# Kernel tuning notes

Hardware: AMD Instinct MI355X
Metric: run time of the kernel (lower is better)

Reference implementation:

```python
import jax, jax.numpy as jnp
import numpy as np

B, S, D, H, O = 64, 512, 1024, 1024, 1024


def setup_inputs() -> dict:
    key = jax.random.key(0)
    ks = jax.random.split(key, 7)
    s_in = 1.0 / np.sqrt(D)
    s_h = 1.0 / np.sqrt(H)
    return {
        "x": jax.random.normal(ks[0], (B, S, D), dtype=jnp.float32),
        # gate order along axis 0: i, f, o, c_candidate
        "Wx": jax.random.uniform(ks[1], (4, H, D), jnp.float32, -s_in, s_in),
        "bx": jax.random.uniform(ks[2], (4, H), jnp.float32, -s_in, s_in),
        "Wh": jax.random.uniform(ks[3], (4, H, H), jnp.float32, -s_h, s_h),
        "bh": jax.random.uniform(ks[4], (4, H), jnp.float32, -s_h, s_h),
        "Wp": jax.random.uniform(ks[5], (O, H), jnp.float32, -s_h, s_h),
        "bp": jax.random.uniform(ks[6], (O,), jnp.float32, -s_h, s_h),
    }


def reference(x, Wx, bx, Wh, bh, Wp, bp):
    b, s, d = x.shape
    h_dim = Wh.shape[-1]
    # Precompute all input-to-hidden gate projections in one big GEMM:
    # equivalent to W_i(x_t)+b, W_f(x_t)+b, W_o(x_t)+b, W_c(x_t)+b per step.
    xg = jnp.einsum('bsd,ghd->sbgh', x, Wx) + bx  # [S, B, 4, H]

    def step(carry, xg_t):
        c, h = carry
        # hidden-to-hidden projections for all 4 gates, fused
        g = xg_t + jnp.einsum('bh,gkh->bgk', h, Wh) + bh  # [B, 4, H]
        i = jax.nn.sigmoid(g[:, 0])
        f = jax.nn.sigmoid(g[:, 1])
        o = jax.nn.sigmoid(g[:, 2])
        c_cand = jnp.tanh(g[:, 3])
        c_new = f * c + i * c_cand
        h_new = o * jnp.tanh(c_new)
        y = h_new @ Wp.T + bp  # [B, O]
        return (c_new, h_new), y

    init = (jnp.zeros((b, h_dim), x.dtype), jnp.zeros((b, h_dim), x.dtype))
    (c, h), ys = jax.lax.scan(step, init, xg)
    outputs = jnp.transpose(ys, (1, 0, 2))  # [B, S, O]
    return outputs, (c, h)
```

## Files before the change

kernel.cpp:

```cpp
#include <hip/hip_runtime.h>


typedef unsigned short u16;
typedef u16   u16x4  __attribute__((ext_vector_type(4)));
typedef u16   u16x8  __attribute__((ext_vector_type(8)));
typedef __bf16 bf16x8 __attribute__((ext_vector_type(8)));
typedef float f32x4  __attribute__((ext_vector_type(4)));

__device__ __forceinline__ u16 f2bf(float x) {
    unsigned u = __float_as_uint(x);
    u = (u + 0x7FFFu + ((u >> 16) & 1u)) >> 16;
    return (u16)u;
}
__device__ __forceinline__ float bf2f(u16 h) {
    return __uint_as_float(((unsigned)h) << 16);
}
__device__ __forceinline__ float fsig(float x) { return 1.f / (1.f + __expf(-x)); }
__device__ __forceinline__ float ftanh(float x) { return 1.f - 2.f / (__expf(2.f * x) + 1.f); }


__global__ void k_convert_x(const float* __restrict__ x, u16* __restrict__ xb) {
    int bi = blockIdx.x;
    int b = bi >> 9, s = bi & 511;
    const float4* src = (const float4*)(x + (size_t)bi * 1024);
    u16* dst = xb + ((size_t)(s * 64 + b)) * 1024;
    int t = threadIdx.x;
    float4 v = src[t];
    u16x4 o; o.x = f2bf(v.x); o.y = f2bf(v.y); o.z = f2bf(v.z); o.w = f2bf(v.w);
    *(u16x4*)(dst + t * 4) = o;
}

__global__ void k_pack_gates(const float* __restrict__ w, u16* __restrict__ wp) {
    int np = blockIdx.x;
    int g = np & 3, k = np >> 2;
    const float4* src = (const float4*)(w + ((size_t)(g * 1024 + k)) * 1024);
    u16* dst = wp + (size_t)np * 1024;
    int t = threadIdx.x;
    float4 v = src[t];
    u16x4 o; o.x = f2bf(v.x); o.y = f2bf(v.y); o.z = f2bf(v.z); o.w = f2bf(v.w);
    *(u16x4*)(dst + t * 4) = o;
}

__global__ void k_f2bf(const float* __restrict__ src, u16* __restrict__ dst, int n) {
    int i = (blockIdx.x * 256 + threadIdx.x) * 4;
    if (i < n) {
        float4 v = *(const float4*)(src + i);
        u16x4 o; o.x = f2bf(v.x); o.y = f2bf(v.y); o.z = f2bf(v.z); o.w = f2bf(v.w);
        *(u16x4*)(dst + i) = o;
    }
}

__global__ void k_bias(const float* __restrict__ bx, const float* __restrict__ bh,
                       float* __restrict__ bias) {
    int np = blockIdx.x * 256 + threadIdx.x;
    int g = np & 3, k = np >> 2;
    bias[np] = bx[g * 1024 + k] + bh[g * 1024 + k];
}

__global__ void k_init(u16* __restrict__ hall0, float* __restrict__ cstate) {
    int i = blockIdx.x * 256 + threadIdx.x;
    hall0[i] = 0;
    cstate[i] = 0.f;
}

__global__ __launch_bounds__(256) void k_gemm64(
    const u16* __restrict__ A, const u16* __restrict__ Bt,
    int K, int N, int mode,
    u16* __restrict__ Cb,
    float* __restrict__ Cf, const float* __restrict__ bp, int S_, int O_) {
    __shared__ u16 As[64 * 72];
    __shared__ u16 Bs[64 * 72];
    int mb = blockIdx.x, nb = blockIdx.y;
    int tid = threadIdx.x, w = tid >> 6, lane = tid & 63;
    f32x4 acc[4] = {};
    int kchunks = K >> 6;
    for (int kc = 0; kc < kchunks; ++kc) {
        int k0 = kc * 64;
#pragma unroll
        for (int r = 0; r < 2; ++r) {
            int c = tid + 256 * r;
            int row = c >> 3, kk = (c & 7) * 8;
            *(u16x8*)(&As[row * 72 + kk]) =
                *(const u16x8*)(A + (size_t)(mb * 64 + row) * K + k0 + kk);
            *(u16x8*)(&Bs[row * 72 + kk]) =
                *(const u16x8*)(Bt + (size_t)(nb * 64 + row) * K + k0 + kk);
        }
        __syncthreads();
#pragma unroll
        for (int kk = 0; kk < 64; kk += 32) {
            bf16x8 a = *(const bf16x8*)(&As[(w * 16 + (lane & 15)) * 72 + kk + (lane >> 4) * 8]);
#pragma unroll
            for (int nt = 0; nt < 4; ++nt) {
                bf16x8 b = *(const bf16x8*)(&Bs[(nt * 16 + (lane & 15)) * 72 + kk + (lane >> 4) * 8]);
                acc[nt] = __builtin_amdgcn_mfma_f32_16x16x32_bf16(a, b, acc[nt], 0, 0, 0);
            }
        }
        __syncthreads();
    }
    int q = lane >> 4, cl = lane & 15;
    if (mode == 0) {
#pragma unroll
        for (int nt = 0; nt < 4; ++nt)
#pragma unroll
            for (int j = 0; j < 4; ++j) {
                int m = mb * 64 + w * 16 + q * 4 + j;
                int n = nb * 64 + nt * 16 + cl;
                Cb[(size_t)m * N + n] = f2bf(acc[nt][j]);
            }
    } else {
#pragma unroll
        for (int nt = 0; nt < 4; ++nt)
#pragma unroll
            for (int j = 0; j < 4; ++j) {
                int m = mb * 64 + w * 16 + q * 4 + j;
                int n = nb * 64 + nt * 16 + cl;
                int b = m & 63, s = m >> 6;
                Cf[((size_t)b * S_ + s) * O_ + n] = acc[nt][j] + bp[n];
            }
    }
}

__global__ __launch_bounds__(256) void k_step(
    const u16* __restrict__ hprev,
    const u16* __restrict__ whp,
    const u16* __restrict__ xgt,
    const float* __restrict__ bias,
    float* __restrict__ cstate,
    float* __restrict__ hf32,
    u16* __restrict__ hnext) {
    __shared__ u16 As[64 * 264];
    __shared__ u16 Bs[16 * 264];
    __shared__ float glds[64 * 20];
    int nb = blockIdx.x;
    int tid = threadIdx.x, w = tid >> 6, lane = tid & 63;
    f32x4 acc = {};
    for (int kc = 0; kc < 4; ++kc) {
        int k0 = kc * 256;
#pragma unroll
        for (int r = 0; r < 8; ++r) {
            int c = tid + 256 * r;
            int row = c >> 5, kk = (c & 31) * 8;
            *(u16x8*)(&As[row * 264 + kk]) =
                *(const u16x8*)(hprev + (size_t)row * 1024 + k0 + kk);
        }
#pragma unroll
        for (int r = 0; r < 2; ++r) {
            int c = tid + 256 * r;
            int row = c >> 5, kk = (c & 31) * 8;
            *(u16x8*)(&Bs[row * 264 + kk]) =
                *(const u16x8*)(whp + (size_t)(nb * 16 + row) * 1024 + k0 + kk);
        }
        __syncthreads();
#pragma unroll
        for (int kk = 0; kk < 256; kk += 32) {
            bf16x8 a = *(const bf16x8*)(&As[(w * 16 + (lane & 15)) * 264 + kk + (lane >> 4) * 8]);
            bf16x8 b = *(const bf16x8*)(&Bs[(lane & 15) * 264 + kk + (lane >> 4) * 8]);
            acc = __builtin_amdgcn_mfma_f32_16x16x32_bf16(a, b, acc, 0, 0, 0);
        }
        __syncthreads();
    }
    int q = lane >> 4, cl = lane & 15;
#pragma unroll
    for (int j = 0; j < 4; ++j) {
        int row = w * 16 + q * 4 + j;
        int n = nb * 16 + cl;
        glds[row * 20 + cl] = acc[j] + bf2f(xgt[(size_t)row * 4096 + n]) + bias[n];
    }
    __syncthreads();
    {
        int row = tid >> 2, kv = tid & 3;
        float4 gv = *(const float4*)(&glds[row * 20 + kv * 4]);
        float ig = fsig(gv.x), fg = fsig(gv.y), og = fsig(gv.z), cc = ftanh(gv.w);
        int k = nb * 4 + kv;
        float c_old = cstate[row * 1024 + k];
        float c_new = fg * c_old + ig * cc;
        cstate[row * 1024 + k] = c_new;
        float h = og * ftanh(c_new);
        hf32[row * 1024 + k] = h;
        hnext[row * 1024 + k] = f2bf(h);
    }
}

__global__ void k_tail(const float* __restrict__ cstate, const float* __restrict__ hf32,
                       float* __restrict__ out) {
    int i = blockIdx.x * 256 + threadIdx.x;
    if (i < 65536) out[33554432 + i] = cstate[i];
    else           out[33554432 + i] = hf32[i - 65536];
}

extern "C" void kernel_launch(void* const* d_in, const int* in_sizes, int n_in,
                              void* d_out, int out_size, void* d_ws, size_t ws_size,
                              hipStream_t stream) {
    const float* x  = (const float*)d_in[0];
    const float* Wx = (const float*)d_in[1];
    const float* bx = (const float*)d_in[2];
    const float* Wh = (const float*)d_in[3];
    const float* bh = (const float*)d_in[4];
    const float* Wp = (const float*)d_in[5];
    const float* bp = (const float*)d_in[6];
    float* out = (float*)d_out;
    char* ws = (char*)d_ws;

    u16*   xb   = (u16*)  (ws);
    u16*   wxp  = (u16*)  (ws + 67108864);
    u16*   whp  = (u16*)  (ws + 75497472);
    u16*   wpb  = (u16*)  (ws + 83886080);
    float* bias = (float*)(ws + 85983232);
    float* cst  = (float*)(ws + 85999616);
    float* hf32 = (float*)(ws + 86261760);
    u16*   xg   = (u16*)  (ws + 86523904);
    u16*   hall = (u16*)  (ws + 354959360);

    k_convert_x<<<32768, 256, 0, stream>>>(x, xb);
    k_pack_gates<<<4096, 256, 0, stream>>>(Wx, wxp);
    k_pack_gates<<<4096, 256, 0, stream>>>(Wh, whp);
    k_f2bf<<<1024, 256, 0, stream>>>(Wp, wpb, 1048576);
    k_bias<<<16, 256, 0, stream>>>(bx, bh, bias);
    k_init<<<256, 256, 0, stream>>>(hall, cst);

    k_gemm64<<<dim3(512, 64), 256, 0, stream>>>(xb, wxp, 1024, 4096, 0,
                                                xg, nullptr, nullptr, 0, 0);
    for (int t = 0; t < 512; ++t) {
        k_step<<<256, 256, 0, stream>>>(hall + (size_t)t * 65536, whp,
                                        xg + (size_t)t * 64 * 4096, bias,
                                        cst, hf32, hall + (size_t)(t + 1) * 65536);
    }
    k_gemm64<<<dim3(512, 16), 256, 0, stream>>>(hall + 65536, wpb, 1024, 1024, 1,
                                                nullptr, out, bp, 512, 1024);
    k_tail<<<512, 256, 0, stream>>>(cst, hf32, out);
}
```

Measured before the change: 4.963 ms.

## Replace per-step LSTM launches with persistent cooperative kernel and grid barrier

Replaces the 512 per-timestep kernel launches with one cooperative persistent kernel of 256 blocks that loops over time and synchronises through a global atomic barrier. Each block keeps its slice of the recurrent weights resident in LDS for the whole run, and cell state stays in registers. The hidden state is read straight from global memory into the MFMA operands instead of being staged through LDS. This removes launch overhead and repeated weight reloads, but adds grid-barrier latency and spin contention on a single counter, and relies on all blocks being co-resident.

```diff
diff --git a/kernel.cpp b/kernel.cpp
--- a/kernel.cpp
+++ b/kernel.cpp
@@ -57,10 +57,12 @@
     bias[np] = bx[g * 1024 + k] + bh[g * 1024 + k];
 }
 
-__global__ void k_init(u16* __restrict__ hall0, float* __restrict__ cstate) {
+__global__ void k_init(u16* __restrict__ hall0, float* __restrict__ cstate,
+                       unsigned* __restrict__ bar) {
     int i = blockIdx.x * 256 + threadIdx.x;
     hall0[i] = 0;
     cstate[i] = 0.f;
+    if (i < 4) bar[i] = 0u;
 }
 
 __global__ __launch_bounds__(256) void k_gemm64(
@@ -120,65 +122,80 @@
     }
 }
 
-__global__ __launch_bounds__(256) void k_step(
-    const u16* __restrict__ hprev,
+__global__ __launch_bounds__(256) void k_recur(
     const u16* __restrict__ whp,
-    const u16* __restrict__ xgt,
+    const u16* __restrict__ xg,
     const float* __restrict__ bias,
-    float* __restrict__ cstate,
+    u16* __restrict__ hall,
+    float* __restrict__ cst,
     float* __restrict__ hf32,
-    u16* __restrict__ hnext) {
-    __shared__ u16 As[64 * 264];
-    __shared__ u16 Bs[16 * 264];
+    unsigned* __restrict__ bar) {
+    __shared__ u16 Bs[16 * 1032];
     __shared__ float glds[64 * 20];
     int nb = blockIdx.x;
     int tid = threadIdx.x, w = tid >> 6, lane = tid & 63;
-    f32x4 acc = {};
-    for (int kc = 0; kc < 4; ++kc) {
-        int k0 = kc * 256;
-#pragma unroll
-        for (int r = 0; r < 8; ++r) {
-            int c = tid + 256 * r;
-            int row = c >> 5, kk = (c & 31) * 8;
-            *(u16x8*)(&As[row * 264 + kk]) =
-                *(const u16x8*)(hprev + (size_t)row * 1024 + k0 + kk);
-        }
-#pragma unroll
-        for (int r = 0; r < 2; ++r) {
-            int c = tid + 256 * r;
-            int row = c >> 5, kk = (c & 31) * 8;
-            *(u16x8*)(&Bs[row * 264 + kk]) =
-                *(const u16x8*)(whp + (size_t)(nb * 16 + row) * 1024 + k0 + kk);
-        }
-        __syncthreads();
-#pragma unroll
-        for (int kk = 0; kk < 256; kk += 32) {
-            bf16x8 a = *(const bf16x8*)(&As[(w * 16 + (lane & 15)) * 264 + kk + (lane >> 4) * 8]);
-            bf16x8 b = *(const bf16x8*)(&Bs[(lane & 15) * 264 + kk + (lane >> 4) * 8]);
+    int q = lane >> 4, cl = lane & 15;
+
+#pragma unroll
+    for (int r = 0; r < 8; ++r) {
+        int c = tid + 256 * r;
+        int row = c >> 7, kk = (c & 127) * 8;
+        *(u16x8*)(&Bs[row * 1032 + kk]) =
+            *(const u16x8*)(whp + (size_t)(nb * 16 + row) * 1024 + kk);
+    }
+    float bcol = bias[nb * 16 + cl];
+    int grow = tid >> 2, gkv = tid & 3;
+    int gk = nb * 4 + gkv;
+    float c_reg = 0.f, h_last = 0.f;
+    __syncthreads();
+
+    for (int t = 0; t < 512; ++t) {
+        const u16* xgt = xg + (size_t)t * 64 * 4096;
+        int row0 = w * 16 + q * 4;
+        int ncol = nb * 16 + cl;
+        u16 xv0 = xgt[(size_t)(row0 + 0) * 4096 + ncol];
+        u16 xv1 = xgt[(size_t)(row0 + 1) * 4096 + ncol];
+        u16 xv2 = xgt[(size_t)(row0 + 2) * 4096 + ncol];
+        u16 xv3 = xgt[(size_t)(row0 + 3) * 4096 + ncol];
+        const u16* hrow = hall + (size_t)t * 65536 + (size_t)(w * 16 + cl) * 1024 + q * 8;
+        f32x4 acc = {};
+#pragma unroll
+        for (int kk = 0; kk < 1024; kk += 32) {
+            bf16x8 a = *(const bf16x8*)(hrow + kk);
+            bf16x8 b = *(const bf16x8*)(&Bs[cl * 1032 + kk + q * 8]);
             acc = __builtin_amdgcn_mfma_f32_16x16x32_bf16(a, b, acc, 0, 0, 0);
         }
-        __syncthreads();
-    }
-    int q = lane >> 4, cl = lane & 15;
-#pragma unroll
-    for (int j = 0; j < 4; ++j) {
-        int row = w * 16 + q * 4 + j;
-        int n = nb * 16 + cl;
-        glds[row * 20 + cl] = acc[j] + bf2f(xgt[(size_t)row * 4096 + n]) + bias[n];
-    }
-    __syncthreads();
-    {
-        int row = tid >> 2, kv = tid & 3;
-        float4 gv = *(const float4*)(&glds[row * 20 + kv * 4]);
+        glds[(row0 + 0) * 20 + cl] = acc[0] + bf2f(xv0) + bcol;
+        glds[(row0 + 1) * 20 + cl] = acc[1] + bf2f(xv1) + bcol;
+        glds[(row0 + 2) * 20 + cl] = acc[2] + bf2f(xv2) + bcol;
+        glds[(row0 + 3) * 20 + cl] = acc[3] + bf2f(xv3) + bcol;
+        __syncthreads();
+        float4 gv = *(const float4*)(&glds[grow * 20 + gkv * 4]);
         float ig = fsig(gv.x), fg = fsig(gv.y), og = fsig(gv.z), cc = ftanh(gv.w);
-        int k = nb * 4 + kv;
-        float c_old = cstate[row * 1024 + k];
-        float c_new = fg * c_old + ig * cc;
-        cstate[row * 1024 + k] = c_new;
-        float h = og * ftanh(c_new);
-        hf32[row * 1024 + k] = h;
-        hnext[row * 1024 + k] = f2bf(h);
-    }
+        c_reg = fg * c_reg + ig * cc;
+        h_last = og * ftanh(c_reg);
+        hall[(size_t)(t + 1) * 65536 + grow * 1024 + gk] = f2bf(h_last);
+        __syncthreads();
+        if (tid == 0) {
+            __builtin_amdgcn_fence(__ATOMIC_RELEASE, "agent");
+            unsigned p = (unsigned)t & 1u;
+            unsigned my = __hip_atomic_fetch_add(&bar[p], 1u, __ATOMIC_ACQ_REL,
+                                                 __HIP_MEMORY_SCOPE_AGENT);
+            if (my == 255u) {
+                __hip_atomic_store(&bar[p], 0u, __ATOMIC_RELAXED,
+                                   __HIP_MEMORY_SCOPE_AGENT);
+                __hip_atomic_fetch_add(&bar[2], 1u, __ATOMIC_RELEASE,
+                                       __HIP_MEMORY_SCOPE_AGENT);
+            } else {
+                while (__hip_atomic_load(&bar[2], __ATOMIC_ACQUIRE,
+                                         __HIP_MEMORY_SCOPE_AGENT) < (unsigned)(t + 1)) {}
+            }
+            __builtin_amdgcn_fence(__ATOMIC_ACQUIRE, "agent");
+        }
+        __syncthreads();
+    }
+    cst[grow * 1024 + gk] = c_reg;
+    hf32[grow * 1024 + gk] = h_last;
 }
 
 __global__ void k_tail(const float* __restrict__ cstate, const float* __restrict__ hf32,
@@ -201,29 +218,31 @@
     float* out = (float*)d_out;
     char* ws = (char*)d_ws;
 
-    u16*   xb   = (u16*)  (ws);
-    u16*   wxp  = (u16*)  (ws + 67108864);
-    u16*   whp  = (u16*)  (ws + 75497472);
-    u16*   wpb  = (u16*)  (ws + 83886080);
-    float* bias = (float*)(ws + 85983232);
-    float* cst  = (float*)(ws + 85999616);
-    float* hf32 = (float*)(ws + 86261760);
-    u16*   xg   = (u16*)  (ws + 86523904);
-    u16*   hall = (u16*)  (ws + 354959360);
+    u16*      xb   = (u16*)     (ws);
+    u16*      wxp  = (u16*)     (ws + 67108864);
+    u16*      whp  = (u16*)     (ws + 75497472);
+    u16*      wpb  = (u16*)     (ws + 83886080);
+    float*    bias = (float*)   (ws + 85983232);
+    float*    cst  = (float*)   (ws + 85999616);
+    float*    hf32 = (float*)   (ws + 86261760);
+    unsigned* bar  = (unsigned*)(ws + 86523648);
+    u16*      xg   = (u16*)     (ws + 86523904);
+    u16*      hall = (u16*)     (ws + 354959360);
 
     k_convert_x<<<32768, 256, 0, stream>>>(x, xb);
     k_pack_gates<<<4096, 256, 0, stream>>>(Wx, wxp);
     k_pack_gates<<<4096, 256, 0, stream>>>(Wh, whp);
     k_f2bf<<<1024, 256, 0, stream>>>(Wp, wpb, 1048576);
     k_bias<<<16, 256, 0, stream>>>(bx, bh, bias);
-    k_init<<<256, 256, 0, stream>>>(hall, cst);
+    k_init<<<256, 256, 0, stream>>>(hall, cst, bar);
 
     k_gemm64<<<dim3(512, 64), 256, 0, stream>>>(xb, wxp, 1024, 4096, 0,
                                                 xg, nullptr, nullptr, 0, 0);
-    for (int t = 0; t < 512; ++t) {
-        k_step<<<256, 256, 0, stream>>>(hall + (size_t)t * 65536, whp,
-                                        xg + (size_t)t * 64 * 4096, bias,
-                                        cst, hf32, hall + (size_t)(t + 1) * 65536);
+    {
+        void* args[] = {(void*)&whp, (void*)&xg, (void*)&bias, (void*)&hall,
+                        (void*)&cst, (void*)&hf32, (void*)&bar};
+        hipLaunchCooperativeKernel((const void*)k_recur, dim3(256), dim3(256),
+                                   args, 0, stream);
     }
     k_gemm64<<<dim3(512, 16), 256, 0, stream>>>(hall + 65536, wpb, 1024, 1024, 1,
                                                 nullptr, out, bp, 512, 1024);
```

Result: slower. 18.00 ms (+262.7%).
